# Kernel optimization log

Measured on AMD Instinct MI355X. Metric: run time of the kernel, lower is better.

Reference implementation:

```python
import jax, jax.numpy as jnp
from jax import lax
import numpy as np

IN_DIM, HID, B, T = 8, 50, 4096, 512

def setup_inputs() -> dict:
    key = jax.random.key(0)
    ks = jax.random.split(key, 8)
    s_ih = 1.0 / np.sqrt(HID)
    return {
        "x": jax.random.normal(ks[0], (B, T, IN_DIM), dtype=jnp.float32),
        "W_ih": jax.random.uniform(ks[1], (3 * HID, IN_DIM), jnp.float32, -s_ih, s_ih),
        "W_hh": jax.random.uniform(ks[2], (3 * HID, HID), jnp.float32, -s_ih, s_ih),
        "b_ih": jax.random.uniform(ks[3], (3 * HID,), jnp.float32, -s_ih, s_ih),
        "b_hh": jax.random.uniform(ks[4], (3 * HID,), jnp.float32, -s_ih, s_ih),
        "W_out": jax.random.uniform(ks[5], (1, HID), jnp.float32, -s_ih, s_ih),
        "b_out": jax.random.uniform(ks[6], (1,), jnp.float32, -s_ih, s_ih),
    }

def reference(x, W_ih, W_hh, b_ih, b_hh, W_out, b_out):
    # Precompute input projections for all timesteps: [B, T, 3H]
    xW = jnp.einsum('bti,gi->btg', x, W_ih) + b_ih

    def step(h, xw_t):  # h: [B, H], xw_t: [B, 3H]
        gi_r, gi_z, gi_n = jnp.split(xw_t, 3, axis=-1)
        gh = h @ W_hh.T + b_hh
        gh_r, gh_z, gh_n = jnp.split(gh, 3, axis=-1)
        r = jax.nn.sigmoid(gi_r + gh_r)
        z = jax.nn.sigmoid(gi_z + gh_z)
        n = jnp.tanh(gi_n + r * gh_n)
        h_new = (1.0 - z) * n + z * h
        return h_new, None

    h0 = jnp.zeros((x.shape[0], W_hh.shape[1]), dtype=x.dtype)
    hT, _ = lax.scan(step, h0, jnp.moveaxis(xW, 1, 0))  # scan over time
    # Linear head on final hidden state; torch squeezes the layer dim -> [B, 1]
    return hT @ W_out.T + b_out
```

## Files before the change

### kernel.cpp

```cpp
#include <hip/hip_runtime.h>

#define HID 50
#define IND 8
#define TLEN 512
#define NB 16
#define CH 128
#define XSTR 1032
#define BSTR 88
#define NTILE 13

typedef _Float16 f16x8 __attribute__((ext_vector_type(8)));
typedef _Float16 f16x4 __attribute__((ext_vector_type(4)));
typedef float f32x4 __attribute__((ext_vector_type(4)));

__device__ __forceinline__ float fast_sigmoid(float v) {
    float e = __builtin_amdgcn_exp2f(-1.44269504f * v);
    return __builtin_amdgcn_rcpf(1.0f + e);
}
__device__ __forceinline__ float fast_tanh(float v) {
    float e = __builtin_amdgcn_exp2f(2.88539008f * v);
    return 1.0f - 2.0f * __builtin_amdgcn_rcpf(e + 1.0f);
}

__global__ __launch_bounds__(512, 2) void gru_mfma4(
    const float* __restrict__ x,
    const float* __restrict__ W_ih,
    const float* __restrict__ W_hh,
    const float* __restrict__ b_ih,
    const float* __restrict__ b_hh,
    const float* __restrict__ W_out,
    const float* __restrict__ b_out,
    float* __restrict__ out)
{
    const int tid  = threadIdx.x;
    const int wave = tid >> 6;
    const int lane = tid & 63;
    const int m16  = lane & 15;
    const int quad = lane >> 4;
    const int bb   = blockIdx.x;

    __shared__ _Float16 x_lds[NB * XSTR];
    __shared__ _Float16 B_lds[2][16 * BSTR];
    __shared__ float    red[NB * 56];

    auto aval = [&](int T, int k) -> float {
        const int R  = 16 * T + m16;
        const int jh = R >> 2;
        const int g  = R & 3;
        if (jh >= HID) return 0.f;
        if (g <= 1) {
            if (k < HID) return W_hh[(g * HID + jh) * HID + k];
            if (k >= 56) return W_ih[(g * HID + jh) * IND + (k - 56)];
            return 0.f;
        }
        if (g == 2) return (k < HID) ? W_hh[(2 * HID + jh) * HID + k] : 0.f;
        return (k >= 56) ? W_ih[(2 * HID + jh) * IND + (k - 56)] : 0.f;
    };

    f16x8 a0[2], a1[2];
    f32x4 bias[2];
    float h[2] = {0.f, 0.f};
#pragma unroll
    for (int tt = 0; tt < 2; ++tt) {
        const int T = wave + 8 * tt;
        if (T < NTILE) {
#pragma unroll
            for (int j = 0; j < 8; ++j) {
                a0[tt][j] = (_Float16)aval(T, quad * 8 + j);
                a1[tt][j] = (_Float16)aval(T, 32 + quad * 8 + j);
            }
            const int jh = 4 * T + quad;
#pragma unroll
            for (int r = 0; r < 4; ++r) {
                float v = 0.f;
                if (jh < HID) {
                    if (r == 0)      v = b_ih[jh] + b_hh[jh];
                    else if (r == 1) v = b_ih[HID + jh] + b_hh[HID + jh];
                    else if (r == 2) v = b_hh[2 * HID + jh];
                    else             v = b_ih[2 * HID + jh];
                }
                bias[tt][r] = v;
            }
        } else {
#pragma unroll
            for (int j = 0; j < 8; ++j) { a0[tt][j] = (_Float16)0.f; a1[tt][j] = (_Float16)0.f; }
            bias[tt] = f32x4{0.f, 0.f, 0.f, 0.f};
        }
    }

    auto stage_chunk = [&](int c) {
        const int n = tid >> 5;
        const int s = tid & 31;
        const float4* src = (const float4*)(x + ((size_t)(bb * NB + n) * TLEN + (size_t)c * CH) * IND);
#pragma unroll
        for (int r = 0; r < 8; ++r) {
            const int fidx = s + 32 * r;
            const float4 v = src[fidx];
            const int trel = fidx >> 1;
            const int d    = (fidx & 1) * 4;
            *(f16x4*)&x_lds[n * XSTR + trel * 8 + d] =
                f16x4{(_Float16)v.x, (_Float16)v.y, (_Float16)v.z, (_Float16)v.w};
        }
    };

    for (int idx = tid; idx < 2 * 16 * BSTR; idx += 512)
        B_lds[0][idx] = (_Float16)0.f;
    stage_chunk(0);
    __syncthreads();

    for (int t = 0; t < TLEN; ++t) {
        const int cur = t & 1, nxt = cur ^ 1;

        if ((t & (CH - 1)) == 0 && t != 0) {
            stage_chunk(t >> 7);
            __syncthreads();
        }

        const f16x8 bf0 = *(const f16x8*)&B_lds[cur][m16 * BSTR + quad * 8];
        const _Float16* bf1p = (quad == 3)
            ? &x_lds[m16 * XSTR + (t & (CH - 1)) * 8]
            : &B_lds[cur][m16 * BSTR + 32 + quad * 8];
        const f16x8 bf1 = *(const f16x8*)bf1p;

        f32x4 c[2];
#pragma unroll
        for (int tt = 0; tt < 2; ++tt) {
            if (wave + 8 * tt < NTILE) {
                c[tt] = __builtin_amdgcn_mfma_f32_16x16x32_f16(a0[tt], bf0, bias[tt], 0, 0, 0);
                c[tt] = __builtin_amdgcn_mfma_f32_16x16x32_f16(a1[tt], bf1, c[tt],   0, 0, 0);
            }
        }

#pragma unroll
        for (int tt = 0; tt < 2; ++tt) {
            const int T = wave + 8 * tt;
            if (T < NTILE) {
                const int jh = 4 * T + quad;
                const float r  = fast_sigmoid(c[tt][0]);
                const float z  = fast_sigmoid(c[tt][1]);
                const float nn = fast_tanh(c[tt][3] + r * c[tt][2]);
                h[tt] = nn + z * (h[tt] - nn);
                if (jh < HID)
                    B_lds[nxt][m16 * BSTR + jh] = (_Float16)h[tt];
            }
        }

        __syncthreads();
    }

#pragma unroll
    for (int tt = 0; tt < 2; ++tt) {
        const int T = wave + 8 * tt;
        if (T < NTILE) {
            const int jh = 4 * T + quad;
            if (jh < HID)
                red[m16 * 56 + jh] = h[tt] * W_out[jh];
        }
    }
    __syncthreads();
    if (tid < NB) {
        float s = b_out[0];
        for (int j = 0; j < HID; ++j) s += red[tid * 56 + j];
        out[bb * NB + tid] = s;
    }
}

extern "C" void kernel_launch(void* const* d_in, const int* in_sizes, int n_in,
                              void* d_out, int out_size, void* d_ws, size_t ws_size,
                              hipStream_t stream) {
    const float* x     = (const float*)d_in[0];
    const float* W_ih  = (const float*)d_in[1];
    const float* W_hh  = (const float*)d_in[2];
    const float* b_ih  = (const float*)d_in[3];
    const float* b_hh  = (const float*)d_in[4];
    const float* W_out = (const float*)d_in[5];
    const float* b_out = (const float*)d_in[6];
    float* out = (float*)d_out;

    const int B = in_sizes[0] / (TLEN * IND);
    gru_mfma4<<<B / NB, 512, 0, stream>>>(x, W_ih, W_hh, b_ih, b_hh, W_out, b_out, out);
}
```

Measured before the change: 289.0 us.

## Use one wave per MFMA tile with 13-wave blocks and independent MFMA accumulators

Blocks grow from 8 to 13 waves so each wave owns exactly one 16-row gate tile, replacing the two-tile-per-wave split where some waves did double work. The two MFMAs per step now accumulate into separate results that are summed afterwards, which removes the dependency between them. The time loop is unrolled by two with fixed buffer indices. In exchange the 832-thread blocks run at one per CU under the new launch bounds, which lowers occupancy, and every step's barrier now synchronises more waves.

```diff
diff --git a/kernel.cpp b/kernel.cpp
--- a/kernel.cpp
+++ b/kernel.cpp
@@ -22,7 +22,7 @@
     return 1.0f - 2.0f * __builtin_amdgcn_rcpf(e + 1.0f);
 }
 
-__global__ __launch_bounds__(512, 2) void gru_mfma4(
+__global__ __launch_bounds__(832, 1) void gru_mfma5(
     const float* __restrict__ x,
     const float* __restrict__ W_ih,
     const float* __restrict__ W_hh,
@@ -38,125 +38,99 @@
     const int m16  = lane & 15;
     const int quad = lane >> 4;
     const int bb   = blockIdx.x;
+    const int jh   = 4 * wave + quad;
 
     __shared__ _Float16 x_lds[NB * XSTR];
     __shared__ _Float16 B_lds[2][16 * BSTR];
     __shared__ float    red[NB * 56];
 
-    auto aval = [&](int T, int k) -> float {
-        const int R  = 16 * T + m16;
-        const int jh = R >> 2;
+    auto aval = [&](int k) -> float {
+        const int R  = 16 * wave + m16;
+        const int rj = R >> 2;
         const int g  = R & 3;
-        if (jh >= HID) return 0.f;
+        if (rj >= HID) return 0.f;
         if (g <= 1) {
-            if (k < HID) return W_hh[(g * HID + jh) * HID + k];
-            if (k >= 56) return W_ih[(g * HID + jh) * IND + (k - 56)];
+            if (k < HID) return W_hh[(g * HID + rj) * HID + k];
+            if (k >= 56) return W_ih[(g * HID + rj) * IND + (k - 56)];
             return 0.f;
         }
-        if (g == 2) return (k < HID) ? W_hh[(2 * HID + jh) * HID + k] : 0.f;
-        return (k >= 56) ? W_ih[(2 * HID + jh) * IND + (k - 56)] : 0.f;
+        if (g == 2) return (k < HID) ? W_hh[(2 * HID + rj) * HID + k] : 0.f;
+        return (k >= 56) ? W_ih[(2 * HID + rj) * IND + (k - 56)] : 0.f;
     };
 
-    f16x8 a0[2], a1[2];
-    f32x4 bias[2];
-    float h[2] = {0.f, 0.f};
+    f16x8 a0, a1;
 #pragma unroll
-    for (int tt = 0; tt < 2; ++tt) {
-        const int T = wave + 8 * tt;
-        if (T < NTILE) {
+    for (int j = 0; j < 8; ++j) {
+        a0[j] = (_Float16)aval(quad * 8 + j);
+        a1[j] = (_Float16)aval(32 + quad * 8 + j);
+    }
+    f32x4 bias;
 #pragma unroll
-            for (int j = 0; j < 8; ++j) {
-                a0[tt][j] = (_Float16)aval(T, quad * 8 + j);
-                a1[tt][j] = (_Float16)aval(T, 32 + quad * 8 + j);
-            }
-            const int jh = 4 * T + quad;
-#pragma unroll
-            for (int r = 0; r < 4; ++r) {
-                float v = 0.f;
-                if (jh < HID) {
-                    if (r == 0)      v = b_ih[jh] + b_hh[jh];
-                    else if (r == 1) v = b_ih[HID + jh] + b_hh[HID + jh];
-                    else if (r == 2) v = b_hh[2 * HID + jh];
-                    else             v = b_ih[2 * HID + jh];
-                }
-                bias[tt][r] = v;
-            }
-        } else {
-#pragma unroll
-            for (int j = 0; j < 8; ++j) { a0[tt][j] = (_Float16)0.f; a1[tt][j] = (_Float16)0.f; }
-            bias[tt] = f32x4{0.f, 0.f, 0.f, 0.f};
+    for (int r = 0; r < 4; ++r) {
+        float v = 0.f;
+        if (jh < HID) {
+            if (r == 0)      v = b_ih[jh] + b_hh[jh];
+            else if (r == 1) v = b_ih[HID + jh] + b_hh[HID + jh];
+            else if (r == 2) v = b_hh[2 * HID + jh];
+            else             v = b_ih[2 * HID + jh];
         }
+        bias[r] = v;
     }
+    const f32x4 zero4 = {0.f, 0.f, 0.f, 0.f};
+    float h = 0.f;
 
     auto stage_chunk = [&](int c) {
-        const int n = tid >> 5;
-        const int s = tid & 31;
-        const float4* src = (const float4*)(x + ((size_t)(bb * NB + n) * TLEN + (size_t)c * CH) * IND);
+        if (tid < 512) {
+            const int n = tid >> 5;
+            const int s = tid & 31;
+            const float4* src = (const float4*)(x + ((size_t)(bb * NB + n) * TLEN + (size_t)c * CH) * IND);
 #pragma unroll
-        for (int r = 0; r < 8; ++r) {
-            const int fidx = s + 32 * r;
-            const float4 v = src[fidx];
-            const int trel = fidx >> 1;
-            const int d    = (fidx & 1) * 4;
-            *(f16x4*)&x_lds[n * XSTR + trel * 8 + d] =
-                f16x4{(_Float16)v.x, (_Float16)v.y, (_Float16)v.z, (_Float16)v.w};
+            for (int r = 0; r < 8; ++r) {
+                const int fidx = s + 32 * r;
+                const float4 v = src[fidx];
+                const int trel = fidx >> 1;
+                const int d    = (fidx & 1) * 4;
+                *(f16x4*)&x_lds[n * XSTR + trel * 8 + d] =
+                    f16x4{(_Float16)v.x, (_Float16)v.y, (_Float16)v.z, (_Float16)v.w};
+            }
         }
     };
 
-    for (int idx = tid; idx < 2 * 16 * BSTR; idx += 512)
+    for (int idx = tid; idx < 2 * 16 * BSTR; idx += 832)
         B_lds[0][idx] = (_Float16)0.f;
     stage_chunk(0);
     __syncthreads();
 
-    for (int t = 0; t < TLEN; ++t) {
-        const int cur = t & 1, nxt = cur ^ 1;
-
-        if ((t & (CH - 1)) == 0 && t != 0) {
-            stage_chunk(t >> 7);
-            __syncthreads();
-        }
-
+    auto step = [&](int t, int cur, int nxt) {
         const f16x8 bf0 = *(const f16x8*)&B_lds[cur][m16 * BSTR + quad * 8];
         const _Float16* bf1p = (quad == 3)
             ? &x_lds[m16 * XSTR + (t & (CH - 1)) * 8]
             : &B_lds[cur][m16 * BSTR + 32 + quad * 8];
         const f16x8 bf1 = *(const f16x8*)bf1p;
 
-        f32x4 c[2];
-#pragma unroll
-        for (int tt = 0; tt < 2; ++tt) {
-            if (wave + 8 * tt < NTILE) {
-                c[tt] = __builtin_amdgcn_mfma_f32_16x16x32_f16(a0[tt], bf0, bias[tt], 0, 0, 0);
-                c[tt] = __builtin_amdgcn_mfma_f32_16x16x32_f16(a1[tt], bf1, c[tt],   0, 0, 0);
-            }
+        const f32x4 c = __builtin_amdgcn_mfma_f32_16x16x32_f16(a0, bf0, bias,  0, 0, 0);
+        const f32x4 d = __builtin_amdgcn_mfma_f32_16x16x32_f16(a1, bf1, zero4, 0, 0, 0);
+
+        const float r  = fast_sigmoid(c[0] + d[0]);
+        const float z  = fast_sigmoid(c[1] + d[1]);
+        const float nn = fast_tanh((c[3] + d[3]) + r * (c[2] + d[2]));
+        h = nn + z * (h - nn);
+        if (jh < HID)
+            B_lds[nxt][m16 * BSTR + jh] = (_Float16)h;
+        __syncthreads();
+    };
+
+    for (int t2 = 0; t2 < TLEN; t2 += 2) {
+        if ((t2 & (CH - 1)) == 0 && t2 != 0) {
+            stage_chunk(t2 >> 7);
+            __syncthreads();
         }
-
-#pragma unroll
-        for (int tt = 0; tt < 2; ++tt) {
-            const int T = wave + 8 * tt;
-            if (T < NTILE) {
-                const int jh = 4 * T + quad;
-                const float r  = fast_sigmoid(c[tt][0]);
-                const float z  = fast_sigmoid(c[tt][1]);
-                const float nn = fast_tanh(c[tt][3] + r * c[tt][2]);
-                h[tt] = nn + z * (h[tt] - nn);
-                if (jh < HID)
-                    B_lds[nxt][m16 * BSTR + jh] = (_Float16)h[tt];
-            }
-        }
-
-        __syncthreads();
+        step(t2,     0, 1);
+        step(t2 + 1, 1, 0);
     }
 
-#pragma unroll
-    for (int tt = 0; tt < 2; ++tt) {
-        const int T = wave + 8 * tt;
-        if (T < NTILE) {
-            const int jh = 4 * T + quad;
-            if (jh < HID)
-                red[m16 * 56 + jh] = h[tt] * W_out[jh];
-        }
-    }
+    if (jh < HID)
+        red[m16 * 56 + jh] = h * W_out[jh];
     __syncthreads();
     if (tid < NB) {
         float s = b_out[0];
@@ -178,5 +152,5 @@
     float* out = (float*)d_out;
 
     const int B = in_sizes[0] / (TLEN * IND);
-    gru_mfma4<<<B / NB, 512, 0, stream>>>(x, W_ih, W_hh, b_ih, b_hh, W_out, b_out, out);
+    gru_mfma5<<<B / NB, 832, 0, stream>>>(x, W_ih, W_hh, b_ih, b_hh, W_out, b_out, out);
 }
```

After: 265.2 us. 8.2% less time.
